# Optimization experiments

Hardware: AMD Instinct MI355X
Metric: run time of the kernel (lower is better)

Reference implementation:

```python
import jax, jax.numpy as jnp
import numpy as np

B, N, C = 4, 4096, 64
K1, K2 = 4, 6
MLP1 = [128, 64, 64]
MLP2 = [128, 64]
EPS = 1e-5


def _sqdist(a, b):
    # a: [B,N,3], b: [B,M,3] -> [B,N,M]
    return (jnp.sum(a * a, -1)[:, :, None] + jnp.sum(b * b, -1)[:, None, :]
            - 2.0 * jnp.einsum('bnc,bmc->bnm', a, b))


def _knn_idx(k, xyz, new_xyz):
    # matches knn_point: topk of -square_distance(new_xyz, xyz)
    _, idx = jax.lax.top_k(-_sqdist(new_xyz, xyz), k)
    return idx  # [B,S,k]


def _gather(points, idx):
    # index_points: points [B,N,C], idx [B,S,K] -> [B,S,K,C]
    return jax.vmap(lambda p, i: p[i])(points, idx)


def _conv_bn_relu(x, w, g, b):
    # 1x1 Conv2d (no bias) + BatchNorm2d (train mode) + ReLU, channels-last
    y = jnp.einsum('bnkc,oc->bnko', x, w)
    m = jnp.mean(y, axis=(0, 1, 2), keepdims=True)
    v = jnp.var(y, axis=(0, 1, 2), keepdims=True)
    return jax.nn.relu((y - m) * jax.lax.rsqrt(v + EPS) * g + b)


def _quat_mul(a, b):
    # Hamilton product, matches mul_q_point ordering
    aw, ax, ay, az = a[..., 0], a[..., 1], a[..., 2], a[..., 3]
    bw, bx, by, bz = b[..., 0], b[..., 1], b[..., 2], b[..., 3]
    return jnp.stack([
        aw * bw - ax * bx - ay * by - az * bz,
        aw * bx + ax * bw + ay * bz - az * by,
        aw * by - ax * bz + ay * bw + az * bx,
        aw * bz + ax * by - ay * bx + az * bw], axis=-1)


def _inv_q(q):
    n2 = jnp.sum(q * q, -1, keepdims=True) + 1e-10
    return jnp.concatenate([q[..., :1], -q[..., 1:]], -1) / n2


def _qrot(q, v):
    # rotate points v [B,M,3] by quaternion q [B,4] via q * (0,v) * q^-1
    vq = jnp.concatenate([jnp.zeros(v.shape[:-1] + (1,), v.dtype), v], -1)
    qb = q[:, None, :]
    return _quat_mul(_quat_mul(qb, vq), _inv_q(q)[:, None, :])[..., 1:]


def setup_inputs() -> dict:
    key = jax.random.key(0)
    ks = jax.random.split(key, 32)

    def rn(i, shape, s=1.0):
        return jax.random.normal(ks[i], shape, jnp.float32) * s

    inp = {
        'pos1': rn(0, (B, N, 3)),
        'pos2': rn(1, (B, N, 3)),
        'feat1': rn(2, (B, N, C)),
        'feat2': rn(3, (B, N, C)),
        'q_coarse': rn(4, (B, 4)),
        't_coarse': rn(5, (B, 3)),
    }
    c1 = [2 * C + 3] + MLP1
    for i in range(len(MLP1)):
        inp['w1_%d' % i] = rn(6 + i, (c1[i + 1], c1[i]), 0.1)
        inp['g1_%d' % i] = jnp.ones((c1[i + 1],), jnp.float32)
        inp['b1_%d' % i] = jnp.zeros((c1[i + 1],), jnp.float32)
    c2 = [MLP1[-1] + C + 3] + MLP2
    for i in range(len(MLP2)):
        inp['w2_%d' % i] = rn(12 + i, (c2[i + 1], c2[i]), 0.1)
        inp['g2_%d' % i] = jnp.ones((c2[i + 1],), jnp.float32)
        inp['b2_%d' % i] = jnp.zeros((c2[i + 1],), jnp.float32)
    inp['wq'] = rn(20, (4, MLP2[-1]), 0.01)
    inp['bq'] = jnp.zeros((4,), jnp.float32)
    inp['wt'] = rn(21, (3, MLP2[-1]), 0.01)
    inp['bt'] = jnp.zeros((3,), jnp.float32)
    return inp


def reference(pos1, pos2, feat1, feat2, q_coarse, t_coarse,
              w1_0, g1_0, b1_0, w1_1, g1_1, b1_1, w1_2, g1_2, b1_2,
              w2_0, g2_0, b2_0, w2_1, g2_1, b2_1, wq, bq, wt, bt):
    # warp pos1 by the coarse pose (q, t)
    pos1_w = _qrot(q_coarse, pos1) + t_coarse[:, None, :]

    # cross-cloud KNN grouping (FlowEmbedding first stage)
    idx2 = _knn_idx(K2, pos2, pos1_w)                      # [B,N,K2]
    xd2 = _gather(pos2, idx2) - pos1_w[:, :, None, :]      # [B,N,K2,3]
    f2g = _gather(feat2, idx2)                             # [B,N,K2,C]
    f1r = jnp.broadcast_to(feat1[:, :, None, :], (B, N, K2, C))
    x = jnp.concatenate([xd2, f2g, f1r], -1)               # [B,N,K2,131]
    for w, g, b in ((w1_0, g1_0, b1_0), (w1_1, g1_1, b1_1), (w1_2, g1_2, b1_2)):
        x = _conv_bn_relu(x, w, g, b)
    fe = jnp.sum(x, axis=2)                                # [B,N,64] sum pool over neighbors

    # self KNN grouping (FlowEmbedding second stage)
    idx1 = _knn_idx(K1, pos1_w, pos1_w)                    # [B,N,K1]
    xd1 = _gather(pos1_w, idx1) - pos1_w[:, :, None, :]
    feg = _gather(fe, idx1)
    f1r2 = jnp.broadcast_to(feat1[:, :, None, :], (B, N, K1, C))
    x = jnp.concatenate([xd1, feg, f1r2], -1)              # [B,N,K1,131]
    for w, g, b in ((w2_0, g2_0, b2_0), (w2_1, g2_1, b2_1)):
        x = _conv_bn_relu(x, w, g, b)
    pooled = jnp.sum(jnp.sum(x, axis=2), axis=1)           # [B,64] sum pool

    # pose delta heads + quaternion composition
    q_det = pooled @ wq.T + bq
    q_det = q_det / (jnp.linalg.norm(q_det, axis=-1, keepdims=True) + 1e-10)
    t_det = pooled @ wt.T + bt
    q_new = _quat_mul(q_det, q_coarse)
    q_new = q_new / (jnp.linalg.norm(q_new, axis=-1, keepdims=True) + 1e-10)
    t_new = _qrot(q_det, t_coarse[:, None, :])[:, 0, :] + t_det
    return jnp.concatenate([q_new, t_new], -1)             # [B,7]
```

## Files before the change

### kernel.cpp

```cpp
#include <hip/hip_runtime.h>
#include <math.h>

#define B_ 4
#define N_ 4096
#define C_ 64
#define K1_ 4
#define K2_ 6
#define EPS_ 1e-5f
#define BN_ (B_ * N_)
#define NCH_ 16
#define CHP_ 256
#define STKD_ 16

typedef __attribute__((ext_vector_type(8))) short bf16x8;
typedef __attribute__((ext_vector_type(4))) float f32x4;
typedef __attribute__((ext_vector_type(2))) float f32x2;

__device__ __forceinline__ unsigned short f2bf(float f) {
  unsigned int u = __float_as_uint(f);
  unsigned int r = (u + 0x7fffu + ((u >> 16) & 1u)) >> 16;
  return (unsigned short)r;
}
__device__ __forceinline__ float bf2f(unsigned short u) {
  return __uint_as_float(((unsigned int)u) << 16);
}

__global__ __launch_bounds__(256) void k_init(
    const float* __restrict__ w1_0, const float* __restrict__ w1_1,
    const float* __restrict__ w1_2, const float* __restrict__ w2_0,
    const float* __restrict__ w2_1, unsigned short* __restrict__ Wf2a,
    unsigned short* __restrict__ Wf1a, unsigned short* __restrict__ Wfe,
    unsigned short* __restrict__ Wf1b, unsigned short* __restrict__ wb1,
    unsigned short* __restrict__ wb2, unsigned short* __restrict__ wb4,
    const float* __restrict__ pos1, const float* __restrict__ pos2,
    const float* __restrict__ qc, const float* __restrict__ tc,
    float* __restrict__ posw, float4* __restrict__ pts4w, float4* __restrict__ pairW,
    float4* __restrict__ pairP, float* __restrict__ zbase) {
  int t = blockIdx.x * 256 + threadIdx.x;
  int m = blockIdx.y;
  if (m < 7) {
    switch (m) {
      case 0:
        if (t < 8192) Wf2a[t] = f2bf(w1_0[(t >> 6) * 131 + 3 + (t & 63)]);
        break;
      case 1:
        if (t < 8192) Wf1a[t] = f2bf(w1_0[(t >> 6) * 131 + 67 + (t & 63)]);
        break;
      case 2:
        if (t < 8192) Wfe[t] = f2bf(w2_0[(t >> 6) * 131 + 3 + (t & 63)]);
        break;
      case 3:
        if (t < 8192) Wf1b[t] = f2bf(w2_0[(t >> 6) * 131 + 67 + (t & 63)]);
        break;
      case 4:
        if (t < 8192) wb1[t] = f2bf(w1_1[t]);
        break;
      case 5:
        if (t < 4096) wb2[t] = f2bf(w1_2[t]);
        break;
      default:
        if (t < 8192) wb4[t] = f2bf(w2_1[t]);
        break;
    }
    return;
  }
  if (m == 8) {
    if (t < 10240) zbase[t] = 0.f;
    return;
  }
  if (t >= BN_) return;
  int b = t / N_;
  float qw = qc[b * 4 + 0], qx = qc[b * 4 + 1], qy = qc[b * 4 + 2], qz = qc[b * 4 + 3];
  float vx = pos1[t * 3 + 0], vy = pos1[t * 3 + 1], vz = pos1[t * 3 + 2];
  float aw = -(qx * vx + qy * vy + qz * vz);
  float ax = qw * vx + qy * vz - qz * vy;
  float ay = qw * vy - qx * vz + qz * vx;
  float az = qw * vz + qx * vy - qy * vx;
  float n2 = qw * qw + qx * qx + qy * qy + qz * qz + 1e-10f;
  float bw = qw / n2, bx = -qx / n2, by = -qy / n2, bz = -qz / n2;
  float rx = aw * bx + ax * bw + ay * bz - az * by;
  float ry = aw * by - ax * bz + ay * bw + az * bx;
  float rz = aw * bz + ax * by - ay * bx + az * bw;
  rx += tc[b * 3 + 0];
  ry += tc[b * 3 + 1];
  rz += tc[b * 3 + 2];
  posw[t * 3 + 0] = rx;
  posw[t * 3 + 1] = ry;
  posw[t * 3 + 2] = rz;
  float rw2 = rx * rx + ry * ry + rz * rz;
  pts4w[t] = make_float4(rx, ry, rz, rw2);
  int p = t >> 1, h = t & 1;
  float* bwp = (float*)&pairW[(size_t)2 * p];
  bwp[0 + h] = rx; bwp[2 + h] = ry; bwp[4 + h] = rz; bwp[6 + h] = rw2;
  float px = pos2[t * 3 + 0], py = pos2[t * 3 + 1], pz = pos2[t * 3 + 2];
  float pw2 = px * px + py * py + pz * pz;
  float* bpp = (float*)&pairP[(size_t)2 * p];
  bpp[0 + h] = px; bpp[2 + h] = py; bpp[4 + h] = pz; bpp[6 + h] = pw2;
}

__device__ __forceinline__ void ins6i(int (&kd)[6], int k) {
  int x = k;
#pragma unroll
  for (int u = 0; u < 6; ++u) {
    int lo = min(kd[u], x);
    x = max(kd[u], x);
    kd[u] = lo;
  }
}

__device__ __forceinline__ void proj_mfma_tail(const unsigned short* Xs, int tid,
                                               int row0,
                                               const unsigned short* __restrict__ Wb,
                                               float* __restrict__ dst) {
  constexpr int SP = 72;
  int l = tid & 63, wv = tid >> 6;
  int lm = l & 15, quad = l >> 4;
  int n0 = wv * 32;
  f32x4 acc[4][2];
#pragma unroll
  for (int rt = 0; rt < 4; ++rt)
#pragma unroll
    for (int ct = 0; ct < 2; ++ct) acc[rt][ct] = (f32x4)(0.f);
#pragma unroll
  for (int k0 = 0; k0 < 64; k0 += 32) {
    bf16x8 a[4], b[2];
#pragma unroll
    for (int rt = 0; rt < 4; ++rt)
      a[rt] = *(const bf16x8*)&Xs[(rt * 16 + lm) * SP + k0 + quad * 8];
#pragma unroll
    for (int ct = 0; ct < 2; ++ct)
      b[ct] = *(const bf16x8*)&Wb[(size_t)(n0 + ct * 16 + lm) * 64 + k0 + quad * 8];
#pragma unroll
    for (int rt = 0; rt < 4; ++rt)
#pragma unroll
      for (int ct = 0; ct < 2; ++ct)
        acc[rt][ct] =
            __builtin_amdgcn_mfma_f32_16x16x32_bf16(a[rt], b[ct], acc[rt][ct], 0, 0, 0);
  }
#pragma unroll
  for (int rt = 0; rt < 4; ++rt)
#pragma unroll
    for (int ct = 0; ct < 2; ++ct)
#pragma unroll
      for (int r = 0; r < 4; ++r) {
        int row = row0 + rt * 16 + quad * 4 + r;
        dst[(size_t)row * 128 + n0 + ct * 16 + lm] = acc[rt][ct][r];
      }
}

__global__ __launch_bounds__(256) void k_knnproj(
    const float4* __restrict__ pts4w, const float4* __restrict__ pairW,
    const float4* __restrict__ pairP, int* __restrict__ outK,
    const float* __restrict__ feat2, const unsigned short* __restrict__ Wf2a,
    float* __restrict__ P2a, const float* __restrict__ feat1,
    const unsigned short* __restrict__ Wf1a, float* __restrict__ P1a,
    const unsigned short* __restrict__ Wf1b, float* __restrict__ P1b) {
  __shared__ int st[STKD_][256];
  int tid = threadIdx.x;
  int bid = blockIdx.x;
  if (bid < 768) {
    const float* src;
    const unsigned short* Wb;
    float* dst;
    switch (bid >> 8) {
      case 0: src = feat2; Wb = Wf2a; dst = P2a; break;
      case 1: src = feat1; Wb = Wf1a; dst = P1a; break;
      default: src = feat1; Wb = Wf1b; dst = P1b; break;
    }
    unsigned short* Xs = (unsigned short*)&st[0][0];
    int row0 = (bid & 255) * 64;
    for (int e = tid; e < 64 * 16; e += 256) {
      int r = e >> 4, s = e & 15;
      float4 v = *(const float4*)&src[(size_t)(row0 + r) * 64 + s * 4];
      ushort4 o;
      o.x = f2bf(v.x); o.y = f2bf(v.y); o.z = f2bf(v.z); o.w = f2bf(v.w);
      *(ushort4*)&Xs[r * 72 + s * 4] = o;
    }
    __syncthreads();
    proj_mfma_tail(Xs, tid, row0, Wb, dst);
    return;
  }
  int kbid = bid - 768;
  int x = kbid & 15, y = (kbid >> 4) & 15, z = kbid >> 8;
  int b = z & 3;
  int which = z >> 2;
  const f32x4* __restrict__ PT =
      (const f32x4*)((which ? pairW : pairP) + (size_t)b * N_ + y * CHP_);
  int base = y * CHP_;
  int n = x * 256 + tid;
  float4 qv = pts4w[(size_t)b * N_ + n];
  f32x2 qq2 = (f32x2)(qv.w);
  f32x2 m2x = (f32x2)(-2.f * qv.x);
  f32x2 m2y = (f32x2)(-2.f * qv.y);
  f32x2 m2z = (f32x2)(-2.f * qv.z);
  int kd[6];
#pragma unroll
  for (int t = 0; t < 6; ++t) kd[t] = 0x7fffffff;
  int kbd5 = 0x7fffffff;
  int ptr = 0;
  for (int jj = 0; jj < CHP_; jj += 4) {
    f32x4 e0 = PT[jj + 0];
    f32x4 e1 = PT[jj + 1];
    f32x4 e2 = PT[jj + 2];
    f32x4 e3 = PT[jj + 3];
    f32x2 d01 = __builtin_elementwise_fma(
        m2x, e0.xy,
        __builtin_elementwise_fma(m2y, e0.zw,
                                  __builtin_elementwise_fma(m2z, e1.xy, e1.zw + qq2)));
    f32x2 d23 = __builtin_elementwise_fma(
        m2x, e2.xy,
        __builtin_elementwise_fma(m2y, e2.zw,
                                  __builtin_elementwise_fma(m2z, e3.xy, e3.zw + qq2)));
    int j0 = base + jj;
    int k0 = (int)((__float_as_uint(d01.x) & 0xFFFFF000u) | (unsigned)(j0 + 0));
    int k1 = (int)((__float_as_uint(d01.y) & 0xFFFFF000u) | (unsigned)(j0 + 1));
    int k2 = (int)((__float_as_uint(d23.x) & 0xFFFFF000u) | (unsigned)(j0 + 2));
    int k3 = (int)((__float_as_uint(d23.y) & 0xFFFFF000u) | (unsigned)(j0 + 3));
    st[ptr][tid] = k0;
    ptr += (k0 < kbd5) ? 1 : 0;
    st[ptr][tid] = k1;
    ptr += (k1 < kbd5) ? 1 : 0;
    st[ptr][tid] = k2;
    ptr += (k2 < kbd5) ? 1 : 0;
    st[ptr][tid] = k3;
    ptr += (k3 < kbd5) ? 1 : 0;
    if (__ballot(ptr >= STKD_ - 4)) {
      for (int i = 0; i < ptr; ++i) ins6i(kd, st[i][tid]);
      ptr = 0;
      kbd5 = kd[5];
    }
  }
  for (int i = 0; i < ptr; ++i) ins6i(kd, st[i][tid]);
  size_t ob = ((size_t)which * BN_ * NCH_ + (size_t)(b * N_ + n) * NCH_ + y) * 6;
#pragma unroll
  for (int t = 0; t < 6; ++t) outK[ob + t] = kd[t];
}

__global__ __launch_bounds__(64) void k_knn2_merge(const int* __restrict__ inK,
                                                   int* __restrict__ idx2,
                                                   int* __restrict__ idx1) {
  int t = blockIdx.x * 64 + threadIdx.x;
  if (t >= 2 * BN_) return;
  int which = (t >= BN_) ? 1 : 0;
  int qi = t - which * BN_;
  int kd[6];
#pragma unroll
  for (int u = 0; u < 6; ++u) kd[u] = 0x7fffffff;
  size_t ib = ((size_t)which * BN_ + qi) * NCH_ * 6;
  for (int c = 0; c < NCH_ * 6; ++c) ins6i(kd, inK[ib + c]);
  if (which) {
#pragma unroll
    for (int u = 0; u < K1_; ++u) idx1[(size_t)qi * K1_ + u] = kd[u] & 0xFFF;
  } else {
#pragma unroll
    for (int u = 0; u < K2_; ++u) idx2[(size_t)qi * K2_ + u] = kd[u] & 0xFFF;
  }
}

__global__ __launch_bounds__(256) void k_feproj(const unsigned short* __restrict__ y3,
                                                const float* __restrict__ stat,
                                                const float* __restrict__ g,
                                                const float* __restrict__ bb,
                                                const unsigned short* __restrict__ Wfe,
                                                float* __restrict__ Pfe) {
  constexpr int SP = 72;
  __shared__ unsigned short Xs[64 * SP];
  __shared__ float scl[C_], shf[C_];
  int tid = threadIdx.x;
  if (tid < C_) {
    int c = tid;
    float s = 0.f, s2 = 0.f;
#pragma unroll
    for (int u = 0; u < 8; ++u) {
      s += stat[c * 8 + u];
      s2 += stat[C_ * 8 + c * 8 + u];
    }
    const float invM = 1.f / (float)(BN_ * K2_);
    float m = s * invM;
    float v = s2 * invM - m * m;
    float sc = g[c] * rsqrtf(v + EPS_);
    scl[c] = sc;
    shf[c] = bb[c] - m * sc;
  }
  __syncthreads();
  int row0 = blockIdx.x * 64;
  for (int e = tid; e < 64 * 16; e += 256) {
    int r = e >> 4, s = e & 15;
    size_t base = ((size_t)(row0 + r) * K2_) * C_ + s * 4;
    float a0 = 0.f, a1 = 0.f, a2 = 0.f, a3 = 0.f;
#pragma unroll
    for (int k = 0; k < K2_; ++k) {
      ushort4 u = *(const ushort4*)&y3[base + (size_t)k * C_];
      a0 += fmaxf(fmaf(bf2f(u.x), scl[s * 4 + 0], shf[s * 4 + 0]), 0.f);
      a1 += fmaxf(fmaf(bf2f(u.y), scl[s * 4 + 1], shf[s * 4 + 1]), 0.f);
      a2 += fmaxf(fmaf(bf2f(u.z), scl[s * 4 + 2], shf[s * 4 + 2]), 0.f);
      a3 += fmaxf(fmaf(bf2f(u.w), scl[s * 4 + 3], shf[s * 4 + 3]), 0.f);
    }
    ushort4 o;
    o.x = f2bf(a0); o.y = f2bf(a1); o.z = f2bf(a2); o.w = f2bf(a3);
    *(ushort4*)&Xs[r * SP + s * 4] = o;
  }
  __syncthreads();
  proj_mfma_tail(Xs, tid, row0, Wfe, Pfe);
}

template <int KNN>
__global__ __launch_bounds__(256) void k_asm(
    const float* __restrict__ Wfull,
    const float* __restrict__ posP, const float* __restrict__ posw,
    const float* __restrict__ Pj, const float* __restrict__ Pn,
    const int* __restrict__ idx, unsigned short* __restrict__ yout,
    float* __restrict__ statOut) {
  __shared__ float Wx[3][128];
  __shared__ float red[16][128];
  int tid = threadIdx.x;
  if (tid < 128) {
    Wx[0][tid] = Wfull[tid * 131 + 0];
    Wx[1][tid] = Wfull[tid * 131 + 1];
    Wx[2][tid] = Wfull[tid * 131 + 2];
  }
  __syncthreads();
  int cg = tid & 15, rg = tid >> 4;
  int c0 = cg * 8;
  int row0 = blockIdx.x * 128 + rg * 8;
  float wx0[8], wx1[8], wx2[8];
#pragma unroll
  for (int u = 0; u < 8; ++u) {
    wx0[u] = Wx[0][c0 + u];
    wx1[u] = Wx[1][c0 + u];
    wx2[u] = Wx[2][c0 + u];
  }
  float s1[8], s2[8];
#pragma unroll
  for (int u = 0; u < 8; ++u) { s1[u] = 0.f; s2[u] = 0.f; }
#pragma unroll
  for (int i = 0; i < 8; ++i) {
    int row = row0 + i;
    int g = row / KNN;
    int bb = g >> 12;
    int j = idx[row];
    int gj = (bb << 12) + j;
    float xd0 = posP[(size_t)gj * 3 + 0] - posw[(size_t)g * 3 + 0];
    float xd1 = posP[(size_t)gj * 3 + 1] - posw[(size_t)g * 3 + 1];
    float xd2 = posP[(size_t)gj * 3 + 2] - posw[(size_t)g * 3 + 2];
    const float* pj = &Pj[(size_t)gj * 128 + c0];
    const float* pn = &Pn[(size_t)g * 128 + c0];
    float4 a0 = *(const float4*)&pj[0];
    float4 a1 = *(const float4*)&pj[4];
    float4 b0 = *(const float4*)&pn[0];
    float4 b1 = *(const float4*)&pn[4];
    float y[8];
    y[0] = a0.x + b0.x; y[1] = a0.y + b0.y; y[2] = a0.z + b0.z; y[3] = a0.w + b0.w;
    y[4] = a1.x + b1.x; y[5] = a1.y + b1.y; y[6] = a1.z + b1.z; y[7] = a1.w + b1.w;
    ushort4 o0, o1;
    unsigned short ob[8];
#pragma unroll
    for (int u = 0; u < 8; ++u) {
      float v = y[u];
      v = fmaf(xd0, wx0[u], v);
      v = fmaf(xd1, wx1[u], v);
      v = fmaf(xd2, wx2[u], v);
      s1[u] += v;
      s2[u] = fmaf(v, v, s2[u]);
      ob[u] = f2bf(v);
    }
    o0.x = ob[0]; o0.y = ob[1]; o0.z = ob[2]; o0.w = ob[3];
    o1.x = ob[4]; o1.y = ob[5]; o1.z = ob[6]; o1.w = ob[7];
    *(ushort4*)&yout[(size_t)row * 128 + c0] = o0;
    *(ushort4*)&yout[(size_t)row * 128 + c0 + 4] = o1;
  }
  int slot = blockIdx.x & 7;
#pragma unroll
  for (int u = 0; u < 8; ++u) red[rg][c0 + u] = s1[u];
  __syncthreads();
  if (tid < 128) {
    float s = 0.f;
#pragma unroll
    for (int r = 0; r < 16; ++r) s += red[r][tid];
    atomicAdd(&statOut[tid * 8 + slot], s);
  }
  __syncthreads();
#pragma unroll
  for (int u = 0; u < 8; ++u) red[rg][c0 + u] = s2[u];
  __syncthreads();
  if (tid < 128) {
    float s = 0.f;
#pragma unroll
    for (int r = 0; r < 16; ++r) s += red[r][tid];
    atomicAdd(&statOut[128 * 8 + tid * 8 + slot], s);
  }
}

template <int CIN, int COUT, int KP>
__global__ __launch_bounds__(256) void k_layer_mfma(
    const unsigned short* __restrict__ Wb,
    const unsigned short* __restrict__ yprev,
    const float* __restrict__ statPrev, const float* __restrict__ gPrev,
    const float* __restrict__ bPrev, float prevInvM,
    unsigned short* __restrict__ yout,
    float* __restrict__ statOut) {
  constexpr int SP = KP + 8;
  constexpr int CST = COUT + 8;
  constexpr int CT = COUT / 64;
  __shared__ unsigned short Xs[64 * SP];
  __shared__ float scl[CIN];
  __shared__ float shf[CIN];

  int tid = threadIdx.x;
  int row0 = blockIdx.x * 64;

  for (int c = tid; c < CIN; c += 256) {
    float s = 0.f, s2 = 0.f;
#pragma unroll
    for (int u = 0; u < 8; ++u) {
      s += statPrev[c * 8 + u];
      s2 += statPrev[CIN * 8 + c * 8 + u];
    }
    float m = s * prevInvM;
    float v = s2 * prevInvM - m * m;
    float sc = gPrev[c] * rsqrtf(v + EPS_);
    scl[c] = sc;
    shf[c] = bPrev[c] - m * sc;
  }
  __syncthreads();
  constexpr int S4 = KP / 4;
  for (int e = tid; e < 64 * S4; e += 256) {
    int r = e / S4, s = e - r * S4;
    int row = row0 + r;
    ushort4 u = *(const ushort4*)&yprev[(size_t)row * CIN + s * 4];
    ushort4 o;
    o.x = f2bf(fmaxf(fmaf(bf2f(u.x), scl[s * 4 + 0], shf[s * 4 + 0]), 0.f));
    o.y = f2bf(fmaxf(fmaf(bf2f(u.y), scl[s * 4 + 1], shf[s * 4 + 1]), 0.f));
    o.z = f2bf(fmaxf(fmaf(bf2f(u.z), scl[s * 4 + 2], shf[s * 4 + 2]), 0.f));
    o.w = f2bf(fmaxf(fmaf(bf2f(u.w), scl[s * 4 + 3], shf[s * 4 + 3]), 0.f));
    *(ushort4*)&Xs[r * SP + s * 4] = o;
  }
  __syncthreads();

  int l = tid & 63, wv = tid >> 6;
  int lm = l & 15, quad = l >> 4;
  int n0 = wv * (COUT / 4);

  f32x4 acc[4][CT];
#pragma unroll
  for (int rt = 0; rt < 4; ++rt)
#pragma unroll
    for (int ct = 0; ct < CT; ++ct) acc[rt][ct] = (f32x4)(0.f);

#pragma unroll
  for (int k0 = 0; k0 < KP; k0 += 32) {
    bf16x8 a[4], b[CT];
#pragma unroll
    for (int rt = 0; rt < 4; ++rt)
      a[rt] = *(const bf16x8*)&Xs[(rt * 16 + lm) * SP + k0 + quad * 8];
#pragma unroll
    for (int ct = 0; ct < CT; ++ct)
      b[ct] = *(const bf16x8*)&Wb[(size_t)(n0 + ct * 16 + lm) * KP + k0 + quad * 8];
#pragma unroll
    for (int rt = 0; rt < 4; ++rt)
#pragma unroll
      for (int ct = 0; ct < CT; ++ct)
        acc[rt][ct] =
            __builtin_amdgcn_mfma_f32_16x16x32_bf16(a[rt], b[ct], acc[rt][ct], 0, 0, 0);
  }

  int slot = blockIdx.x & 7;
#pragma unroll
  for (int ct = 0; ct < CT; ++ct) {
    float s1 = 0.f, s2 = 0.f;
#pragma unroll
    for (int rt = 0; rt < 4; ++rt)
#pragma unroll
      for (int r = 0; r < 4; ++r) {
        float v = acc[rt][ct][r];
        s1 += v;
        s2 += v * v;
      }
    s1 += __shfl_xor(s1, 16);
    s1 += __shfl_xor(s1, 32);
    s2 += __shfl_xor(s2, 16);
    s2 += __shfl_xor(s2, 32);
    if (quad == 0) {
      int col = n0 + ct * 16 + lm;
      atomicAdd(&statOut[col * 8 + slot], s1);
      atomicAdd(&statOut[COUT * 8 + col * 8 + slot], s2);
    }
  }

  __syncthreads();
  unsigned short* Ys = Xs;
#pragma unroll
  for (int rt = 0; rt < 4; ++rt)
#pragma unroll
    for (int ct = 0; ct < CT; ++ct)
#pragma unroll
      for (int r = 0; r < 4; ++r)
        Ys[(rt * 16 + quad * 4 + r) * CST + n0 + ct * 16 + lm] = f2bf(acc[rt][ct][r]);
  __syncthreads();
  constexpr int S8 = COUT / 8;
  for (int e = tid; e < 64 * S8; e += 256) {
    int r = e / S8, c0 = (e - r * S8) * 8;
    uint4 v = *(const uint4*)&Ys[r * CST + c0];
    *(uint4*)&yout[((size_t)(row0 + r)) * COUT + c0] = v;
  }
}

__global__ __launch_bounds__(256) void k_pooled(const unsigned short* __restrict__ y5,
                                                const float* __restrict__ stat,
                                                const float* __restrict__ g,
                                                const float* __restrict__ bb,
                                                float* __restrict__ pooled) {
  __shared__ float scl[C_], shf[C_];
  __shared__ float red[4][C_];
  if (threadIdx.x < C_) {
    int c = threadIdx.x;
    float s = 0.f, s2 = 0.f;
#pragma unroll
    for (int u = 0; u < 8; ++u) {
      s += stat[c * 8 + u];
      s2 += stat[C_ * 8 + c * 8 + u];
    }
    const float invM = 1.f / (float)(BN_ * K1_);
    float m = s * invM;
    float v = s2 * invM - m * m;
    float sc = g[c] * rsqrtf(v + EPS_);
    scl[c] = sc;
    shf[c] = bb[c] - m * sc;
  }
  __syncthreads();
  int c = threadIdx.x & 63;
  int rs = threadIdx.x >> 6;
  int row0 = blockIdx.x * 64;
  int b = row0 / (N_ * K1_);
  float s = 0.f;
  for (int i = 0; i < 16; ++i) {
    int row = row0 + rs * 16 + i;
    s += fmaxf(fmaf(bf2f(y5[(size_t)row * C_ + c]), scl[c], shf[c]), 0.f);
  }
  red[rs][c] = s;
  __syncthreads();
  if (threadIdx.x < C_) {
    float t2 = red[0][c] + red[1][c] + red[2][c] + red[3][c];
    atomicAdd(&pooled[(b * C_ + c) * 8 + (blockIdx.x & 7)], t2);
  }
}

__global__ void k_final(const float* __restrict__ pooled, const float* __restrict__ wq,
                        const float* __restrict__ bq, const float* __restrict__ wt,
                        const float* __restrict__ bt, const float* __restrict__ qc,
                        const float* __restrict__ tc, float* __restrict__ out) {
  int b = threadIdx.x;
  if (b >= B_) return;
  float P[C_];
#pragma unroll
  for (int c = 0; c < C_; ++c) {
    float s = 0.f;
#pragma unroll
    for (int u = 0; u < 8; ++u) s += pooled[(b * C_ + c) * 8 + u];
    P[c] = s;
  }
  float qd[4];
#pragma unroll
  for (int i = 0; i < 4; ++i) {
    float s = bq[i];
#pragma unroll
    for (int c = 0; c < C_; ++c) s = fmaf(P[c], wq[i * C_ + c], s);
    qd[i] = s;
  }
  float td[3];
#pragma unroll
  for (int i = 0; i < 3; ++i) {
    float s = bt[i];
#pragma unroll
    for (int c = 0; c < C_; ++c) s = fmaf(P[c], wt[i * C_ + c], s);
    td[i] = s;
  }
  float nq = sqrtf(qd[0] * qd[0] + qd[1] * qd[1] + qd[2] * qd[2] + qd[3] * qd[3]) + 1e-10f;
#pragma unroll
  for (int i = 0; i < 4; ++i) qd[i] /= nq;
  float cw = qc[b * 4 + 0], cx = qc[b * 4 + 1], cyy = qc[b * 4 + 2], cz = qc[b * 4 + 3];
  float qnw = qd[0] * cw - qd[1] * cx - qd[2] * cyy - qd[3] * cz;
  float qnx = qd[0] * cx + qd[1] * cw + qd[2] * cz - qd[3] * cyy;
  float qny = qd[0] * cyy - qd[1] * cz + qd[2] * cw + qd[3] * cx;
  float qnz = qd[0] * cz + qd[1] * cyy - qd[2] * cx + qd[3] * cw;
  float nn = sqrtf(qnw * qnw + qnx * qnx + qny * qny + qnz * qnz) + 1e-10f;
  float vx = tc[b * 3 + 0], vy = tc[b * 3 + 1], vz = tc[b * 3 + 2];
  float aw = -(qd[1] * vx + qd[2] * vy + qd[3] * vz);
  float ax = qd[0] * vx + qd[2] * vz - qd[3] * vy;
  float ay = qd[0] * vy - qd[1] * vz + qd[3] * vx;
  float az = qd[0] * vz + qd[1] * vy - qd[2] * vx;
  float n2 = qd[0] * qd[0] + qd[1] * qd[1] + qd[2] * qd[2] + qd[3] * qd[3] + 1e-10f;
  float bw = qd[0] / n2, bx = -qd[1] / n2, by = -qd[2] / n2, bz = -qd[3] / n2;
  float rx = aw * bx + ax * bw + ay * bz - az * by;
  float ry = aw * by - ax * bz + ay * bw + az * bx;
  float rz = aw * bz + ax * by - ay * bx + az * bw;
  out[b * 7 + 0] = qnw / nn;
  out[b * 7 + 1] = qnx / nn;
  out[b * 7 + 2] = qny / nn;
  out[b * 7 + 3] = qnz / nn;
  out[b * 7 + 4] = rx + td[0];
  out[b * 7 + 5] = ry + td[1];
  out[b * 7 + 6] = rz + td[2];
}

extern "C" void kernel_launch(void* const* d_in, const int* in_sizes, int n_in,
                              void* d_out, int out_size, void* d_ws, size_t ws_size,
                              hipStream_t stream) {
  const float* pos1 = (const float*)d_in[0];
  const float* pos2 = (const float*)d_in[1];
  const float* feat1 = (const float*)d_in[2];
  const float* feat2 = (const float*)d_in[3];
  const float* qc = (const float*)d_in[4];
  const float* tc = (const float*)d_in[5];
  const float* w1_0 = (const float*)d_in[6];
  const float* g1_0 = (const float*)d_in[7];
  const float* b1_0 = (const float*)d_in[8];
  const float* w1_1 = (const float*)d_in[9];
  const float* g1_1 = (const float*)d_in[10];
  const float* b1_1 = (const float*)d_in[11];
  const float* w1_2 = (const float*)d_in[12];
  const float* g1_2 = (const float*)d_in[13];
  const float* b1_2 = (const float*)d_in[14];
  const float* w2_0 = (const float*)d_in[15];
  const float* g2_0 = (const float*)d_in[16];
  const float* b2_0 = (const float*)d_in[17];
  const float* w2_1 = (const float*)d_in[18];
  const float* g2_1 = (const float*)d_in[19];
  const float* b2_1 = (const float*)d_in[20];
  const float* wq = (const float*)d_in[21];
  const float* bq = (const float*)d_in[22];
  const float* wt = (const float*)d_in[23];
  const float* bt = (const float*)d_in[24];

  float* ws = (float*)d_ws;
  const size_t off_posw = 0;
  const size_t off_stat = 49152;
  const size_t off_pool = 57344;
  const size_t off_idx2 = 59392;
  const size_t off_idx1 = 157696;
  const size_t off_wb = 223232;
  const size_t off_pts4w = 249856;
  const size_t off_pairW = 315392;
  const size_t off_pairP = 380928;
  const size_t off_P2a = 446464;
  const size_t off_P1a = 2543616;
  const size_t off_P1b = 4640768;
  const size_t off_Pfe = 6737920;
  const size_t off_yA = 8835072;
  const size_t off_yB = 15126528;

  float* posw = ws + off_posw;
  float* stat0 = ws + off_stat;
  float* stat1 = stat0 + 2048;
  float* stat2 = stat1 + 1024;
  float* stat3 = stat2 + 1024;
  float* stat4 = stat3 + 2048;
  float* pooled = ws + off_pool;
  int* idx2 = (int*)(ws + off_idx2);
  int* idx1 = (int*)(ws + off_idx1);
  unsigned short* Wf2a = (unsigned short*)(ws + off_wb);
  unsigned short* Wf1a = Wf2a + 8192;
  unsigned short* Wfe = Wf1a + 8192;
  unsigned short* Wf1b = Wfe + 8192;
  unsigned short* wb1 = Wf1b + 8192;
  unsigned short* wb2 = wb1 + 8192;
  unsigned short* wb4 = wb2 + 4096;
  float4* pts4w = (float4*)(ws + off_pts4w);
  float4* pairW = (float4*)(ws + off_pairW);
  float4* pairP = (float4*)(ws + off_pairP);
  float* P2a = ws + off_P2a;
  float* P1a = ws + off_P1a;
  float* P1b = ws + off_P1b;
  float* Pfe = ws + off_Pfe;
  unsigned short* yA = (unsigned short*)(ws + off_yA);
  unsigned short* yB = (unsigned short*)(ws + off_yB);
  int* knnK = (int*)yA;

  k_init<<<dim3(64, 9), 256, 0, stream>>>(w1_0, w1_1, w1_2, w2_0, w2_1, Wf2a, Wf1a,
                                          Wfe, Wf1b, wb1, wb2, wb4, pos1, pos2, qc, tc,
                                          posw, pts4w, pairW, pairP, ws + off_stat);

  k_knnproj<<<dim3(768 + 2048), 256, 0, stream>>>(pts4w, pairW, pairP, knnK, feat2,
                                                  Wf2a, P2a, feat1, Wf1a, P1a, Wf1b,
                                                  P1b);
  k_knn2_merge<<<dim3(2 * BN_ / 64), 64, 0, stream>>>(knnK, idx2, idx1);

  k_asm<K2_><<<dim3(98304 / 128), 256, 0, stream>>>(w1_0, pos2, posw, P2a, P1a, idx2,
                                                    yA, stat0);
  k_layer_mfma<128, 64, 128><<<dim3(1536), 256, 0, stream>>>(
      wb1, yA, stat0, g1_0, b1_0, 1.f / 98304.f, yB, stat1);
  k_layer_mfma<64, 64, 64><<<dim3(1536), 256, 0, stream>>>(
      wb2, yB, stat1, g1_1, b1_1, 1.f / 98304.f, yA, stat2);
  k_feproj<<<dim3(256), 256, 0, stream>>>(yA, stat2, g1_2, b1_2, Wfe, Pfe);
  k_asm<K1_><<<dim3(65536 / 128), 256, 0, stream>>>(w2_0, posw, posw, Pfe, P1b, idx1,
                                                    yA, stat3);
  k_layer_mfma<128, 64, 128><<<dim3(1024), 256, 0, stream>>>(
      wb4, yA, stat3, g2_0, b2_0, 1.f / 65536.f, yB, stat4);
  k_pooled<<<dim3(65536 / 64), 256, 0, stream>>>(yB, stat4, g2_1, b2_1, pooled);
  k_final<<<dim3(1), 64, 0, stream>>>(pooled, wq, bq, wt, bt, qc, tc, (float*)d_out);
}
```

Before: 383.8 us.

## Fuse KNN merge into assembly kernels, specialize self-KNN to K=4, widen loads

```diff
diff --git a/kernel.cpp b/kernel.cpp
--- a/kernel.cpp
+++ b/kernel.cpp
@@ -25,6 +25,17 @@
   return __uint_as_float(((unsigned int)u) << 16);
 }
 
+template <int K>
+__device__ __forceinline__ void insKi(int* kd, int k) {
+  int x = k;
+#pragma unroll
+  for (int u = 0; u < K; ++u) {
+    int lo = min(kd[u], x);
+    x = max(kd[u], x);
+    kd[u] = lo;
+  }
+}
+
 __global__ __launch_bounds__(256) void k_init(
     const float* __restrict__ w1_0, const float* __restrict__ w1_1,
     const float* __restrict__ w1_2, const float* __restrict__ w2_0,
@@ -34,8 +45,9 @@
     unsigned short* __restrict__ wb2, unsigned short* __restrict__ wb4,
     const float* __restrict__ pos1, const float* __restrict__ pos2,
     const float* __restrict__ qc, const float* __restrict__ tc,
-    float* __restrict__ posw, float4* __restrict__ pts4w, float4* __restrict__ pairW,
-    float4* __restrict__ pairP, float* __restrict__ zbase) {
+    float4* __restrict__ pts4w, float4* __restrict__ pts4p,
+    float4* __restrict__ pairW, float4* __restrict__ pairP,
+    float* __restrict__ zbase) {
   int t = blockIdx.x * 256 + threadIdx.x;
   int m = blockIdx.y;
   if (m < 7) {
@@ -84,9 +96,6 @@
   rx += tc[b * 3 + 0];
   ry += tc[b * 3 + 1];
   rz += tc[b * 3 + 2];
-  posw[t * 3 + 0] = rx;
-  posw[t * 3 + 1] = ry;
-  posw[t * 3 + 2] = rz;
   float rw2 = rx * rx + ry * ry + rz * rz;
   pts4w[t] = make_float4(rx, ry, rz, rw2);
   int p = t >> 1, h = t & 1;
@@ -94,18 +103,9 @@
   bwp[0 + h] = rx; bwp[2 + h] = ry; bwp[4 + h] = rz; bwp[6 + h] = rw2;
   float px = pos2[t * 3 + 0], py = pos2[t * 3 + 1], pz = pos2[t * 3 + 2];
   float pw2 = px * px + py * py + pz * pz;
+  pts4p[t] = make_float4(px, py, pz, pw2);
   float* bpp = (float*)&pairP[(size_t)2 * p];
   bpp[0 + h] = px; bpp[2 + h] = py; bpp[4 + h] = pz; bpp[6 + h] = pw2;
-}
-
-__device__ __forceinline__ void ins6i(int (&kd)[6], int k) {
-  int x = k;
-#pragma unroll
-  for (int u = 0; u < 6; ++u) {
-    int lo = min(kd[u], x);
-    x = max(kd[u], x);
-    kd[u] = lo;
-  }
 }
 
 __device__ __forceinline__ void proj_mfma_tail(const unsigned short* Xs, int tid,
@@ -148,55 +148,18 @@
       }
 }
 
-__global__ __launch_bounds__(256) void k_knnproj(
-    const float4* __restrict__ pts4w, const float4* __restrict__ pairW,
-    const float4* __restrict__ pairP, int* __restrict__ outK,
-    const float* __restrict__ feat2, const unsigned short* __restrict__ Wf2a,
-    float* __restrict__ P2a, const float* __restrict__ feat1,
-    const unsigned short* __restrict__ Wf1a, float* __restrict__ P1a,
-    const unsigned short* __restrict__ Wf1b, float* __restrict__ P1b) {
-  __shared__ int st[STKD_][256];
-  int tid = threadIdx.x;
-  int bid = blockIdx.x;
-  if (bid < 768) {
-    const float* src;
-    const unsigned short* Wb;
-    float* dst;
-    switch (bid >> 8) {
-      case 0: src = feat2; Wb = Wf2a; dst = P2a; break;
-      case 1: src = feat1; Wb = Wf1a; dst = P1a; break;
-      default: src = feat1; Wb = Wf1b; dst = P1b; break;
-    }
-    unsigned short* Xs = (unsigned short*)&st[0][0];
-    int row0 = (bid & 255) * 64;
-    for (int e = tid; e < 64 * 16; e += 256) {
-      int r = e >> 4, s = e & 15;
-      float4 v = *(const float4*)&src[(size_t)(row0 + r) * 64 + s * 4];
-      ushort4 o;
-      o.x = f2bf(v.x); o.y = f2bf(v.y); o.z = f2bf(v.z); o.w = f2bf(v.w);
-      *(ushort4*)&Xs[r * 72 + s * 4] = o;
-    }
-    __syncthreads();
-    proj_mfma_tail(Xs, tid, row0, Wb, dst);
-    return;
-  }
-  int kbid = bid - 768;
-  int x = kbid & 15, y = (kbid >> 4) & 15, z = kbid >> 8;
-  int b = z & 3;
-  int which = z >> 2;
-  const f32x4* __restrict__ PT =
-      (const f32x4*)((which ? pairW : pairP) + (size_t)b * N_ + y * CHP_);
-  int base = y * CHP_;
-  int n = x * 256 + tid;
-  float4 qv = pts4w[(size_t)b * N_ + n];
+template <int K>
+__device__ __forceinline__ void knn_chunk(const f32x4* __restrict__ PT, int base,
+                                          float4 qv, int tid, int (*st)[256],
+                                          int* __restrict__ orow) {
   f32x2 qq2 = (f32x2)(qv.w);
   f32x2 m2x = (f32x2)(-2.f * qv.x);
   f32x2 m2y = (f32x2)(-2.f * qv.y);
   f32x2 m2z = (f32x2)(-2.f * qv.z);
-  int kd[6];
-#pragma unroll
-  for (int t = 0; t < 6; ++t) kd[t] = 0x7fffffff;
-  int kbd5 = 0x7fffffff;
+  int kd[K];
+#pragma unroll
+  for (int t = 0; t < K; ++t) kd[t] = 0x7fffffff;
+  int kbd = 0x7fffffff;
   int ptr = 0;
   for (int jj = 0; jj < CHP_; jj += 4) {
     f32x4 e0 = PT[jj + 0];
@@ -217,44 +180,70 @@
     int k2 = (int)((__float_as_uint(d23.x) & 0xFFFFF000u) | (unsigned)(j0 + 2));
     int k3 = (int)((__float_as_uint(d23.y) & 0xFFFFF000u) | (unsigned)(j0 + 3));
     st[ptr][tid] = k0;
-    ptr += (k0 < kbd5) ? 1 : 0;
+    ptr += (k0 < kbd) ? 1 : 0;
     st[ptr][tid] = k1;
-    ptr += (k1 < kbd5) ? 1 : 0;
+    ptr += (k1 < kbd) ? 1 : 0;
     st[ptr][tid] = k2;
-    ptr += (k2 < kbd5) ? 1 : 0;
+    ptr += (k2 < kbd) ? 1 : 0;
     st[ptr][tid] = k3;
-    ptr += (k3 < kbd5) ? 1 : 0;
+    ptr += (k3 < kbd) ? 1 : 0;
     if (__ballot(ptr >= STKD_ - 4)) {
-      for (int i = 0; i < ptr; ++i) ins6i(kd, st[i][tid]);
+      for (int i = 0; i < ptr; ++i) insKi<K>(kd, st[i][tid]);
       ptr = 0;
-      kbd5 = kd[5];
-    }
-  }
-  for (int i = 0; i < ptr; ++i) ins6i(kd, st[i][tid]);
-  size_t ob = ((size_t)which * BN_ * NCH_ + (size_t)(b * N_ + n) * NCH_ + y) * 6;
-#pragma unroll
-  for (int t = 0; t < 6; ++t) outK[ob + t] = kd[t];
-}
-
-__global__ __launch_bounds__(64) void k_knn2_merge(const int* __restrict__ inK,
-                                                   int* __restrict__ idx2,
-                                                   int* __restrict__ idx1) {
-  int t = blockIdx.x * 64 + threadIdx.x;
-  if (t >= 2 * BN_) return;
-  int which = (t >= BN_) ? 1 : 0;
-  int qi = t - which * BN_;
-  int kd[6];
-#pragma unroll
-  for (int u = 0; u < 6; ++u) kd[u] = 0x7fffffff;
-  size_t ib = ((size_t)which * BN_ + qi) * NCH_ * 6;
-  for (int c = 0; c < NCH_ * 6; ++c) ins6i(kd, inK[ib + c]);
-  if (which) {
-#pragma unroll
-    for (int u = 0; u < K1_; ++u) idx1[(size_t)qi * K1_ + u] = kd[u] & 0xFFF;
-  } else {
-#pragma unroll
-    for (int u = 0; u < K2_; ++u) idx2[(size_t)qi * K2_ + u] = kd[u] & 0xFFF;
-  }
+      kbd = kd[K - 1];
+    }
+  }
+  for (int i = 0; i < ptr; ++i) insKi<K>(kd, st[i][tid]);
+#pragma unroll
+  for (int t = 0; t < K; ++t) orow[t] = kd[t];
+}
+
+__global__ __launch_bounds__(256) void k_knnproj(
+    const float4* __restrict__ pts4w, const float4* __restrict__ pairW,
+    const float4* __restrict__ pairP, int* __restrict__ outK,
+    const float* __restrict__ feat2, const unsigned short* __restrict__ Wf2a,
+    float* __restrict__ P2a, const float* __restrict__ feat1,
+    const unsigned short* __restrict__ Wf1a, float* __restrict__ P1a,
+    const unsigned short* __restrict__ Wf1b, float* __restrict__ P1b) {
+  __shared__ int st[STKD_][256];
+  int tid = threadIdx.x;
+  int bid = blockIdx.x;
+  if (bid < 768) {
+    const float* src;
+    const unsigned short* Wb;
+    float* dst;
+    switch (bid >> 8) {
+      case 0: src = feat2; Wb = Wf2a; dst = P2a; break;
+      case 1: src = feat1; Wb = Wf1a; dst = P1a; break;
+      default: src = feat1; Wb = Wf1b; dst = P1b; break;
+    }
+    unsigned short* Xs = (unsigned short*)&st[0][0];
+    int row0 = (bid & 255) * 64;
+    for (int e = tid; e < 64 * 16; e += 256) {
+      int r = e >> 4, s = e & 15;
+      float4 v = *(const float4*)&src[(size_t)(row0 + r) * 64 + s * 4];
+      ushort4 o;
+      o.x = f2bf(v.x); o.y = f2bf(v.y); o.z = f2bf(v.z); o.w = f2bf(v.w);
+      *(ushort4*)&Xs[r * 72 + s * 4] = o;
+    }
+    __syncthreads();
+    proj_mfma_tail(Xs, tid, row0, Wb, dst);
+    return;
+  }
+  int kbid = bid - 768;
+  int x = kbid & 15, y = (kbid >> 4) & 15, z = kbid >> 8;
+  int b = z & 3;
+  int which = z >> 2;
+  const f32x4* __restrict__ PT =
+      (const f32x4*)((which ? pairW : pairP) + (size_t)b * N_ + y * CHP_);
+  int base = y * CHP_;
+  int n = x * 256 + tid;
+  float4 qv = pts4w[(size_t)b * N_ + n];
+  int* orow = &outK[((size_t)which * BN_ * NCH_ + (size_t)(b * N_ + n) * NCH_ + y) * 6];
+  if (which == 0)
+    knn_chunk<6>(PT, base, qv, tid, st, orow);
+  else
+    knn_chunk<4>(PT, base, qv, tid, st, orow);
 }
 
 __global__ __launch_bounds__(256) void k_feproj(const unsigned short* __restrict__ y3,
@@ -307,22 +296,41 @@
 template <int KNN>
 __global__ __launch_bounds__(256) void k_asm(
     const float* __restrict__ Wfull,
-    const float* __restrict__ posP, const float* __restrict__ posw,
+    const float4* __restrict__ nbrPts, const float4* __restrict__ qryPts,
     const float* __restrict__ Pj, const float* __restrict__ Pn,
-    const int* __restrict__ idx, unsigned short* __restrict__ yout,
-    float* __restrict__ statOut) {
+    const int* __restrict__ outK,
+    unsigned short* __restrict__ yout, float* __restrict__ statOut) {
   __shared__ float Wx[3][128];
   __shared__ float red[16][128];
+  __shared__ int idxL[33][6];
   int tid = threadIdx.x;
+  int row0 = blockIdx.x * 128;
+  int first = row0 / KNN;
+  int nq = (row0 + 127) / KNN - first + 1;
   if (tid < 128) {
     Wx[0][tid] = Wfull[tid * 131 + 0];
     Wx[1][tid] = Wfull[tid * 131 + 1];
     Wx[2][tid] = Wfull[tid * 131 + 2];
   }
+  if (tid < nq) {
+    int q = first + tid;
+    int km[6];
+#pragma unroll
+    for (int u = 0; u < 6; ++u) km[u] = 0x7fffffff;
+    size_t ib = (size_t)q * (NCH_ * 6);
+    if (KNN == 6) {
+      for (int c = 0; c < NCH_ * 6; ++c) insKi<6>(km, outK[ib + c]);
+    } else {
+      for (int ch = 0; ch < NCH_; ++ch)
+#pragma unroll
+        for (int u = 0; u < 4; ++u) insKi<4>(km, outK[ib + ch * 6 + u]);
+    }
+#pragma unroll
+    for (int u = 0; u < KNN; ++u) idxL[tid][u] = km[u] & 0xFFF;
+  }
   __syncthreads();
   int cg = tid & 15, rg = tid >> 4;
   int c0 = cg * 8;
-  int row0 = blockIdx.x * 128 + rg * 8;
   float wx0[8], wx1[8], wx2[8];
 #pragma unroll
   for (int u = 0; u < 8; ++u) {
@@ -335,14 +343,15 @@
   for (int u = 0; u < 8; ++u) { s1[u] = 0.f; s2[u] = 0.f; }
 #pragma unroll
   for (int i = 0; i < 8; ++i) {
-    int row = row0 + i;
+    int row = row0 + rg * 8 + i;
     int g = row / KNN;
-    int bb = g >> 12;
-    int j = idx[row];
-    int gj = (bb << 12) + j;
-    float xd0 = posP[(size_t)gj * 3 + 0] - posw[(size_t)g * 3 + 0];
-    float xd1 = posP[(size_t)gj * 3 + 1] - posw[(size_t)g * 3 + 1];
-    float xd2 = posP[(size_t)gj * 3 + 2] - posw[(size_t)g * 3 + 2];
+    int j = idxL[g - first][row - g * KNN];
+    int gj = ((g >> 12) << 12) + j;
+    float4 pw = qryPts[g];
+    float4 pn4 = nbrPts[gj];
+    float xd0 = pn4.x - pw.x;
+    float xd1 = pn4.y - pw.y;
+    float xd2 = pn4.z - pw.z;
     const float* pj = &Pj[(size_t)gj * 128 + c0];
     const float* pn = &Pn[(size_t)g * 128 + c0];
     float4 a0 = *(const float4*)&pj[0];
@@ -423,17 +432,24 @@
     shf[c] = bPrev[c] - m * sc;
   }
   __syncthreads();
-  constexpr int S4 = KP / 4;
-  for (int e = tid; e < 64 * S4; e += 256) {
-    int r = e / S4, s = e - r * S4;
+  constexpr int S8 = KP / 8;
+  for (int e = tid; e < 64 * S8; e += 256) {
+    int r = e / S8, s = e - r * S8;
     int row = row0 + r;
-    ushort4 u = *(const ushort4*)&yprev[(size_t)row * CIN + s * 4];
-    ushort4 o;
-    o.x = f2bf(fmaxf(fmaf(bf2f(u.x), scl[s * 4 + 0], shf[s * 4 + 0]), 0.f));
-    o.y = f2bf(fmaxf(fmaf(bf2f(u.y), scl[s * 4 + 1], shf[s * 4 + 1]), 0.f));
-    o.z = f2bf(fmaxf(fmaf(bf2f(u.z), scl[s * 4 + 2], shf[s * 4 + 2]), 0.f));
-    o.w = f2bf(fmaxf(fmaf(bf2f(u.w), scl[s * 4 + 3], shf[s * 4 + 3]), 0.f));
-    *(ushort4*)&Xs[r * SP + s * 4] = o;
+    uint4 u = *(const uint4*)&yprev[(size_t)row * CIN + s * 8];
+    uint4 o;
+    unsigned* up = (unsigned*)&u;
+    unsigned* op = (unsigned*)&o;
+#pragma unroll
+    for (int w = 0; w < 4; ++w) {
+      int c = s * 8 + w * 2;
+      float lo = __uint_as_float(up[w] << 16);
+      float hi = __uint_as_float(up[w] & 0xFFFF0000u);
+      float rl = fmaxf(fmaf(lo, scl[c], shf[c]), 0.f);
+      float rh = fmaxf(fmaf(hi, scl[c + 1], shf[c + 1]), 0.f);
+      op[w] = (unsigned)f2bf(rl) | ((unsigned)f2bf(rh) << 16);
+    }
+    *(uint4*)&Xs[r * SP + s * 8] = o;
   }
   __syncthreads();
 
@@ -497,9 +513,9 @@
       for (int r = 0; r < 4; ++r)
         Ys[(rt * 16 + quad * 4 + r) * CST + n0 + ct * 16 + lm] = f2bf(acc[rt][ct][r]);
   __syncthreads();
-  constexpr int S8 = COUT / 8;
-  for (int e = tid; e < 64 * S8; e += 256) {
-    int r = e / S8, c0 = (e - r * S8) * 8;
+  constexpr int SO = COUT / 8;
+  for (int e = tid; e < 64 * SO; e += 256) {
+    int r = e / SO, c0 = (e - r * SO) * 8;
     uint4 v = *(const uint4*)&Ys[r * CST + c0];
     *(uint4*)&yout[((size_t)(row0 + r)) * COUT + c0] = v;
   }
@@ -511,7 +527,7 @@
                                                 const float* __restrict__ bb,
                                                 float* __restrict__ pooled) {
   __shared__ float scl[C_], shf[C_];
-  __shared__ float red[4][C_];
+  __shared__ float red[16][C_];
   if (threadIdx.x < C_) {
     int c = threadIdx.x;
     float s = 0.f, s2 = 0.f;
@@ -528,20 +544,30 @@
     shf[c] = bb[c] - m * sc;
   }
   __syncthreads();
-  int c = threadIdx.x & 63;
-  int rs = threadIdx.x >> 6;
+  int cq = threadIdx.x & 15, rr = threadIdx.x >> 4;
+  int c0 = cq * 4;
   int row0 = blockIdx.x * 64;
-  int b = row0 / (N_ * K1_);
-  float s = 0.f;
-  for (int i = 0; i < 16; ++i) {
-    int row = row0 + rs * 16 + i;
-    s += fmaxf(fmaf(bf2f(y5[(size_t)row * C_ + c]), scl[c], shf[c]), 0.f);
-  }
-  red[rs][c] = s;
+  int b = blockIdx.x >> 8;
+  float a0 = 0.f, a1 = 0.f, a2 = 0.f, a3 = 0.f;
+#pragma unroll
+  for (int i = 0; i < 4; ++i) {
+    int row = row0 + rr * 4 + i;
+    ushort4 u = *(const ushort4*)&y5[(size_t)row * C_ + c0];
+    a0 += fmaxf(fmaf(bf2f(u.x), scl[c0 + 0], shf[c0 + 0]), 0.f);
+    a1 += fmaxf(fmaf(bf2f(u.y), scl[c0 + 1], shf[c0 + 1]), 0.f);
+    a2 += fmaxf(fmaf(bf2f(u.z), scl[c0 + 2], shf[c0 + 2]), 0.f);
+    a3 += fmaxf(fmaf(bf2f(u.w), scl[c0 + 3], shf[c0 + 3]), 0.f);
+  }
+  red[rr][c0 + 0] = a0;
+  red[rr][c0 + 1] = a1;
+  red[rr][c0 + 2] = a2;
+  red[rr][c0 + 3] = a3;
   __syncthreads();
   if (threadIdx.x < C_) {
-    float t2 = red[0][c] + red[1][c] + red[2][c] + red[3][c];
-    atomicAdd(&pooled[(b * C_ + c) * 8 + (blockIdx.x & 7)], t2);
+    float s = 0.f;
+#pragma unroll
+    for (int r = 0; r < 16; ++r) s += red[r][threadIdx.x];
+    atomicAdd(&pooled[(b * C_ + threadIdx.x) * 8 + (blockIdx.x & 7)], s);
   }
 }
 
@@ -633,31 +659,27 @@
   const float* bt = (const float*)d_in[24];
 
   float* ws = (float*)d_ws;
-  const size_t off_posw = 0;
-  const size_t off_stat = 49152;
-  const size_t off_pool = 57344;
-  const size_t off_idx2 = 59392;
-  const size_t off_idx1 = 157696;
-  const size_t off_wb = 223232;
-  const size_t off_pts4w = 249856;
-  const size_t off_pairW = 315392;
-  const size_t off_pairP = 380928;
-  const size_t off_P2a = 446464;
-  const size_t off_P1a = 2543616;
-  const size_t off_P1b = 4640768;
-  const size_t off_Pfe = 6737920;
-  const size_t off_yA = 8835072;
-  const size_t off_yB = 15126528;
-
-  float* posw = ws + off_posw;
+  const size_t off_stat = 0;
+  const size_t off_pool = 8192;
+  const size_t off_wb = 10240;
+  const size_t off_pts4w = 36864;
+  const size_t off_pts4p = 102400;
+  const size_t off_pairW = 167936;
+  const size_t off_pairP = 233472;
+  const size_t off_knnK = 299008;
+  const size_t off_P2a = 3444736;
+  const size_t off_P1a = 5541888;
+  const size_t off_P1b = 7639040;
+  const size_t off_Pfe = 9736192;
+  const size_t off_yA = 11833344;
+  const size_t off_yB = 18124800;
+
   float* stat0 = ws + off_stat;
   float* stat1 = stat0 + 2048;
   float* stat2 = stat1 + 1024;
   float* stat3 = stat2 + 1024;
   float* stat4 = stat3 + 2048;
   float* pooled = ws + off_pool;
-  int* idx2 = (int*)(ws + off_idx2);
-  int* idx1 = (int*)(ws + off_idx1);
   unsigned short* Wf2a = (unsigned short*)(ws + off_wb);
   unsigned short* Wf1a = Wf2a + 8192;
   unsigned short* Wfe = Wf1a + 8192;
@@ -666,34 +688,34 @@
   unsigned short* wb2 = wb1 + 8192;
   unsigned short* wb4 = wb2 + 4096;
   float4* pts4w = (float4*)(ws + off_pts4w);
+  float4* pts4p = (float4*)(ws + off_pts4p);
   float4* pairW = (float4*)(ws + off_pairW);
   float4* pairP = (float4*)(ws + off_pairP);
+  int* knnK = (int*)(ws + off_knnK);
   float* P2a = ws + off_P2a;
   float* P1a = ws + off_P1a;
   float* P1b = ws + off_P1b;
   float* Pfe = ws + off_Pfe;
   unsigned short* yA = (unsigned short*)(ws + off_yA);
   unsigned short* yB = (unsigned short*)(ws + off_yB);
-  int* knnK = (int*)yA;
 
   k_init<<<dim3(64, 9), 256, 0, stream>>>(w1_0, w1_1, w1_2, w2_0, w2_1, Wf2a, Wf1a,
                                           Wfe, Wf1b, wb1, wb2, wb4, pos1, pos2, qc, tc,
-                                          posw, pts4w, pairW, pairP, ws + off_stat);
+                                          pts4w, pts4p, pairW, pairP, ws + off_stat);
 
   k_knnproj<<<dim3(768 + 2048), 256, 0, stream>>>(pts4w, pairW, pairP, knnK, feat2,
                                                   Wf2a, P2a, feat1, Wf1a, P1a, Wf1b,
                                                   P1b);
-  k_knn2_merge<<<dim3(2 * BN_ / 64), 64, 0, stream>>>(knnK, idx2, idx1);
-
-  k_asm<K2_><<<dim3(98304 / 128), 256, 0, stream>>>(w1_0, pos2, posw, P2a, P1a, idx2,
+
+  k_asm<K2_><<<dim3(98304 / 128), 256, 0, stream>>>(w1_0, pts4p, pts4w, P2a, P1a, knnK,
                                                     yA, stat0);
   k_layer_mfma<128, 64, 128><<<dim3(1536), 256, 0, stream>>>(
       wb1, yA, stat0, g1_0, b1_0, 1.f / 98304.f, yB, stat1);
   k_layer_mfma<64, 64, 64><<<dim3(1536), 256, 0, stream>>>(
       wb2, yB, stat1, g1_1, b1_1, 1.f / 98304.f, yA, stat2);
   k_feproj<<<dim3(256), 256, 0, stream>>>(yA, stat2, g1_2, b1_2, Wfe, Pfe);
-  k_asm<K1_><<<dim3(65536 / 128), 256, 0, stream>>>(w2_0, posw, posw, Pfe, P1b, idx1,
-                                                    yA, stat3);
+  k_asm<K1_><<<dim3(65536 / 128), 256, 0, stream>>>(
+      w2_0, pts4w, pts4w, Pfe, P1b, knnK + (size_t)BN_ * NCH_ * 6, yA, stat3);
   k_layer_mfma<128, 64, 128><<<dim3(1024), 256, 0, stream>>>(
       wb4, yA, stat3, g2_0, b2_0, 1.f / 65536.f, yB, stat4);
   k_pooled<<<dim3(65536 / 64), 256, 0, stream>>>(yB, stat4, g2_1, b2_1, pooled);
```

Result: no change. 382.0 us (-0.5%).
